# Kernel tuning notes

Measured on AMD Instinct MI355X. Metric: run time of the kernel, lower is better.

The kernel has to match this reference:

```python
import jax, jax.numpy as jnp
import numpy as np

B, S, H, NH = 2, 4096, 768, 12
DH = H // NH  # 64


def setup_inputs() -> dict:
    key = jax.random.key(0)
    ks = jax.random.split(key, 7)
    scale = 0.02
    return {
        "x": jax.random.normal(ks[0], (B, S, H), dtype=jnp.float32),
        "Wq": jax.random.normal(ks[1], (H, H), dtype=jnp.float32) * scale,
        "bq": jax.random.normal(ks[2], (H,), dtype=jnp.float32) * scale,
        "Wk": jax.random.normal(ks[3], (H, H), dtype=jnp.float32) * scale,
        "bk": jax.random.normal(ks[4], (H,), dtype=jnp.float32) * scale,
        "Wv": jax.random.normal(ks[5], (H, H), dtype=jnp.float32) * scale,
        "bv": jax.random.normal(ks[6], (H,), dtype=jnp.float32) * scale,
    }


def _split_heads(t):
    # [B,S,H] -> [B,NH,S,DH]
    return t.reshape(B, S, NH, DH).transpose(0, 2, 1, 3)


def reference(x, Wq, bq, Wk, bk, Wv, bv):
    q = _split_heads(x @ Wq + bq)
    k = _split_heads(x @ Wk + bk)
    v = _split_heads(x @ Wv + bv)
    # raw scores + zero additive mask (mask is all zeros, so it is a no-op)
    scores = jnp.einsum("bhqd,bhkd->bhqk", q, k) / jnp.sqrt(jnp.float32(DH))
    probs = jax.nn.softmax(scores, axis=-1)
    ctx = jnp.einsum("bhqk,bhkd->bhqd", probs, v)
    out = ctx.transpose(0, 2, 1, 3).reshape(B, S, H)
    return jnp.tanh(out)
```

## Files before the change

kernel.cpp:

```cpp
#include <hip/hip_runtime.h>
#include <hip/hip_bf16.h>

#define B_ 2
#define S_ 4096
#define H_ 768
#define NH_ 12
#define DH_ 64
#define M_ (B_ * S_)
#define N3_ (3 * H_)
#define NQK 1536
#define K_ H_
#define LOG2E 1.4426950408889634f

typedef __attribute__((ext_vector_type(8))) short short8;
typedef __attribute__((ext_vector_type(4))) float f32x4;
typedef __attribute__((ext_vector_type(16))) float f32x16;
typedef __attribute__((ext_vector_type(4))) unsigned int uint4v;
typedef __attribute__((ext_vector_type(4))) unsigned short ushort4v;

typedef __attribute__((address_space(3))) unsigned int lds_u32;
typedef const __attribute__((address_space(1))) unsigned int glb_u32;

__device__ __forceinline__ unsigned short f2bf(float f) {
    unsigned int u = __builtin_bit_cast(unsigned int, f);
    u += 0x7FFFu + ((u >> 16) & 1u);
    return (unsigned short)(u >> 16);
}
__device__ __forceinline__ unsigned int cvtpk_bf16(float lo, float hi) {
    unsigned int r;
    asm("v_cvt_pk_bf16_f32 %0, %1, %2" : "=v"(r) : "v"(lo), "v"(hi));
    return r;
}
__device__ __forceinline__ void plswap32(unsigned int &x, unsigned int &y) {
    asm("v_permlane32_swap_b32 %0, %1" : "+v"(x), "+v"(y));
}
__device__ __forceinline__ float exp2_fast(float x) {
    float r;
    asm("v_exp_f32 %0, %1" : "=v"(r) : "v"(x));
    return r;
}

__global__ __launch_bounds__(256) void cast_x_kernel(const float* __restrict__ x,
                                                     unsigned short* __restrict__ xb) {
    int i = blockIdx.x * 256 + threadIdx.x;
    float4 v = reinterpret_cast<const float4*>(x)[i];
    ushort4 o;
    o.x = f2bf(v.x); o.y = f2bf(v.y); o.z = f2bf(v.z); o.w = f2bf(v.w);
    reinterpret_cast<ushort4*>(xb)[i] = o;
}

__global__ __launch_bounds__(256) void cast_w_kernel(const float* __restrict__ Wq,
                                                     const float* __restrict__ Wk,
                                                     const float* __restrict__ Wv,
                                                     unsigned short* __restrict__ wt) {
    int id = blockIdx.x * 256 + threadIdx.x;
    int n = id % H_;
    int kb = (id / H_) % 96;
    int wsel = id / (H_ * 96);
    const float* W = (wsel == 0) ? Wq : (wsel == 1) ? Wk : Wv;
    union { unsigned short s[8]; uint4v v; } u;
#pragma unroll
    for (int j = 0; j < 8; j++) u.s[j] = f2bf(W[(size_t)(kb * 8 + j) * H_ + n]);
    *reinterpret_cast<uint4v*>(wt + (size_t)(wsel * H_ + n) * H_ + kb * 8) = u.v;
}

#define GBM 128
#define GBN 128
#define GBK 64

__global__ __launch_bounds__(256) void qkv_gemm_kernel(const unsigned short* __restrict__ xb,
                                                       const unsigned short* __restrict__ wt,
                                                       const float* __restrict__ bq,
                                                       const float* __restrict__ bk,
                                                       const float* __restrict__ bv,
                                                       unsigned short* __restrict__ qk,
                                                       unsigned short* __restrict__ vT) {
    __shared__ unsigned short Asm[GBM * GBK];
    __shared__ unsigned short Bsm[GBN * GBK];
    const int tid = threadIdx.x;
    const int swz = (blockIdx.x & 7) * 144 + (blockIdx.x >> 3);
    const int bm = swz / 18, bn = swz % 18;
    const int w = tid >> 6, l = tid & 63;
    const int wm = w >> 1, wn = w & 1;
    const int lr = l & 15, lk = l >> 4;

    f32x4 zero = {0.f, 0.f, 0.f, 0.f};
    f32x4 acc[4][4];
#pragma unroll
    for (int i = 0; i < 4; i++)
#pragma unroll
        for (int j = 0; j < 4; j++) acc[i][j] = zero;

    const int srow = l >> 3;
    const int scol = (l & 7) * 8;
    const unsigned short* aBase = xb + (size_t)(bm * GBM) * K_;
    const unsigned short* bBase = wt + (size_t)(bn * GBN) * K_;

    for (int k0 = 0; k0 < K_; k0 += GBK) {
        __syncthreads();
#pragma unroll
        for (int i = 0; i < 4; i++) {
            const int j = w * 4 + i;
            __builtin_amdgcn_global_load_lds(
                (glb_u32*)(aBase + (size_t)(j * 8 + srow) * K_ + k0 + scol),
                (lds_u32*)(&Asm[j * 8 * GBK]), 16, 0, 0);
        }
#pragma unroll
        for (int i = 0; i < 4; i++) {
            const int j = w * 4 + i;
            __builtin_amdgcn_global_load_lds(
                (glb_u32*)(bBase + (size_t)(j * 8 + srow) * K_ + k0 + scol),
                (lds_u32*)(&Bsm[j * 8 * GBK]), 16, 0, 0);
        }
        __syncthreads();

#pragma unroll
        for (int ks = 0; ks < 2; ks++) {
            short8 a[4], b[4];
#pragma unroll
            for (int mi = 0; mi < 4; mi++)
                a[mi] = *reinterpret_cast<const short8*>(&Asm[(wm * 64 + mi * 16 + lr) * GBK + ks * 32 + lk * 8]);
#pragma unroll
            for (int ni = 0; ni < 4; ni++)
                b[ni] = *reinterpret_cast<const short8*>(&Bsm[(wn * 64 + ni * 16 + lr) * GBK + ks * 32 + lk * 8]);
#pragma unroll
            for (int mi = 0; mi < 4; mi++)
#pragma unroll
                for (int ni = 0; ni < 4; ni++)
                    acc[mi][ni] = __builtin_amdgcn_mfma_f32_16x16x32_bf16(a[mi], b[ni], acc[mi][ni], 0, 0, 0);
        }
    }

    if (bn < 12) {
#pragma unroll
        for (int ni = 0; ni < 4; ni++) {
            const int col = bn * GBN + wn * 64 + ni * 16 + lr;
            const bool isQ = (col < H_);
            const float bias = isQ ? bq[col] : bk[col - H_];
            const float scl = isQ ? (0.125f * LOG2E) : 1.0f;
#pragma unroll
            for (int mi = 0; mi < 4; mi++) {
#pragma unroll
                for (int i = 0; i < 4; i++) {
                    const int row = bm * GBM + wm * 64 + mi * 16 + lk * 4 + i;
                    qk[(size_t)row * NQK + col] = f2bf((acc[mi][ni][i] + bias) * scl);
                }
            }
        }
    } else {
#pragma unroll
        for (int ni = 0; ni < 4; ni++) {
            const int c = bn * GBN - 2 * H_ + wn * 64 + ni * 16 + lr;
            const int h = c >> 6, d = c & 63;
            const float bias = bv[c];
#pragma unroll
            for (int mi = 0; mi < 4; mi++) {
                const int row0 = bm * GBM + wm * 64 + mi * 16 + lk * 4;
                const int b = row0 >> 12, s0 = row0 & (S_ - 1);
                union { unsigned short s[4]; ushort4v v; } u;
#pragma unroll
                for (int i = 0; i < 4; i++) u.s[i] = f2bf(acc[mi][ni][i] + bias);
                *reinterpret_cast<ushort4v*>(vT + ((size_t)(b * NH_ + h) * DH_ + d) * S_ + s0) = u.v;
            }
        }
    }
}

#define QW 32
#define QB 128
#define KB 64

__global__ __launch_bounds__(256, 2) void attn_kernel(const unsigned short* __restrict__ qk,
                                                      const unsigned short* __restrict__ vT,
                                                      float* __restrict__ out) {
    __shared__ unsigned short Ksm[KB * 64];
    __shared__ unsigned short Vsm[DH_ * KB];
    const int tid = threadIdx.x;
    const int w = tid >> 6, l = tid & 63;
    const int ln = l & 31, hi = l >> 5;
    const int swz = (blockIdx.x & 7) * 96 + (blockIdx.x >> 3);
    const int qt = swz & 31, bh = swz >> 5;
    const int b = bh / NH_, h = bh % NH_;

    const unsigned short* Qg = qk + (size_t)b * S_ * NQK + h * DH_;
    const unsigned short* Kg = Qg + H_;
    const unsigned short* Vg = vT + (size_t)bh * DH_ * S_;

    const int qrow = qt * QB + w * QW + ln;
    short8 qf[4];
    {
        const unsigned short* qp = Qg + (size_t)qrow * NQK + hi * 8;
#pragma unroll
        for (int dk = 0; dk < 4; dk++)
            qf[dk] = *reinterpret_cast<const short8*>(qp + dk * 16);
    }

    const f32x16 fz = {0,0,0,0,0,0,0,0,0,0,0,0,0,0,0,0};
    f32x16 o0 = fz, o1 = fz;
    float m_ = -INFINITY, lsum = 0.f;

    const int srow = tid >> 2;
    const int sd = (tid & 3) * 16;
    const unsigned short* kgp = Kg + (size_t)srow * NQK + sd;
    const unsigned short* vgp = Vg + (size_t)srow * S_ + sd;
    const int sidx0 = (srow * 64 + sd) ^ ((srow & 7) << 3);
    const int sidx1 = (srow * 64 + sd + 8) ^ ((srow & 7) << 3);

    uint4v kr0 = *reinterpret_cast<const uint4v*>(kgp);
    uint4v kr1 = *reinterpret_cast<const uint4v*>(kgp + 8);
    uint4v vr0 = *reinterpret_cast<const uint4v*>(vgp);
    uint4v vr1 = *reinterpret_cast<const uint4v*>(vgp + 8);

    for (int kt = 0; kt < S_; kt += KB) {
        asm volatile("" ::: "memory");
        __builtin_amdgcn_s_barrier();
        asm volatile("" ::: "memory");
        *reinterpret_cast<uint4v*>(&Ksm[sidx0]) = kr0;
        *reinterpret_cast<uint4v*>(&Ksm[sidx1]) = kr1;
        *reinterpret_cast<uint4v*>(&Vsm[sidx0]) = vr0;
        *reinterpret_cast<uint4v*>(&Vsm[sidx1]) = vr1;
        if (kt + KB < S_) {
            kr0 = *reinterpret_cast<const uint4v*>(kgp + (size_t)(kt + KB) * NQK);
            kr1 = *reinterpret_cast<const uint4v*>(kgp + (size_t)(kt + KB) * NQK + 8);
            vr0 = *reinterpret_cast<const uint4v*>(vgp + kt + KB);
            vr1 = *reinterpret_cast<const uint4v*>(vgp + kt + KB + 8);
        }
        asm volatile("s_waitcnt lgkmcnt(0)" ::: "memory");
        __builtin_amdgcn_s_barrier();
        asm volatile("" ::: "memory");

        f32x16 s0 = fz, s1 = fz;
#pragma unroll
        for (int dk = 0; dk < 4; dk++) {
            const int col = dk * 16 + hi * 8;
            short8 kf0 = *reinterpret_cast<const short8*>(&Ksm[(ln * 64 + col) ^ ((ln & 7) << 3)]);
            short8 kf1 = *reinterpret_cast<const short8*>(&Ksm[((32 + ln) * 64 + col) ^ ((ln & 7) << 3)]);
            s0 = __builtin_amdgcn_mfma_f32_32x32x16_bf16(kf0, qf[dk], s0, 0, 0, 0);
            s1 = __builtin_amdgcn_mfma_f32_32x32x16_bf16(kf1, qf[dk], s1, 0, 0, 0);
        }

        float pmax = fmaxf(fmaxf(s0[0], s0[1]), fmaxf(s0[2], s0[3]));
#pragma unroll
        for (int r = 4; r < 16; r += 4)
            pmax = fmaxf(pmax, fmaxf(fmaxf(s0[r], s0[r+1]), fmaxf(s0[r+2], s0[r+3])));
#pragma unroll
        for (int r = 0; r < 16; r += 4)
            pmax = fmaxf(pmax, fmaxf(fmaxf(s1[r], s1[r+1]), fmaxf(s1[r+2], s1[r+3])));
        pmax = fmaxf(pmax, __shfl_xor(pmax, 32));
        if (!__all(pmax - m_ <= 8.0f)) {
            const float mnew = fmaxf(m_, pmax);
            const float corr = exp2_fast(m_ - mnew);
            m_ = mnew;
            lsum *= corr;
#pragma unroll
            for (int r = 0; r < 16; r++) {
                const float c = __shfl(corr, (r & 3) + 8 * (r >> 2) + 4 * hi);
                o0[r] *= c; o1[r] *= c;
            }
        }
        float p[32];
        float rs = 0.f;
#pragma unroll
        for (int r = 0; r < 16; r++) { p[r] = exp2_fast(s0[r] - m_); rs += p[r]; }
#pragma unroll
        for (int r = 0; r < 16; r++) { p[16 + r] = exp2_fast(s1[r] - m_); rs += p[16 + r]; }
        rs += __shfl_xor(rs, 32);
        lsum += rs;

        short8 pa[4];
#pragma unroll
        for (int half = 0; half < 2; half++) {
            unsigned int c0 = cvtpk_bf16(p[half*16+0],  p[half*16+1]);
            unsigned int c1 = cvtpk_bf16(p[half*16+2],  p[half*16+3]);
            unsigned int c2 = cvtpk_bf16(p[half*16+4],  p[half*16+5]);
            unsigned int c3 = cvtpk_bf16(p[half*16+6],  p[half*16+7]);
            unsigned int c4 = cvtpk_bf16(p[half*16+8],  p[half*16+9]);
            unsigned int c5 = cvtpk_bf16(p[half*16+10], p[half*16+11]);
            unsigned int c6 = cvtpk_bf16(p[half*16+12], p[half*16+13]);
            unsigned int c7 = cvtpk_bf16(p[half*16+14], p[half*16+15]);
            plswap32(c0, c2); plswap32(c1, c3);
            plswap32(c4, c6); plswap32(c5, c7);
            union { unsigned int u[4]; short8 v; } ua, ub;
            ua.u[0] = c0; ua.u[1] = c1; ua.u[2] = c2; ua.u[3] = c3;
            ub.u[0] = c4; ub.u[1] = c5; ub.u[2] = c6; ub.u[3] = c7;
            pa[half * 2]     = ua.v;
            pa[half * 2 + 1] = ub.v;
        }

#pragma unroll
        for (int s4 = 0; s4 < 4; s4++) {
            const int kcol = s4 * 16 + hi * 8;
            short8 vf0 = *reinterpret_cast<const short8*>(&Vsm[(ln * 64 + kcol) ^ ((ln & 7) << 3)]);
            short8 vf1 = *reinterpret_cast<const short8*>(&Vsm[((32 + ln) * 64 + kcol) ^ ((ln & 7) << 3)]);
            o0 = __builtin_amdgcn_mfma_f32_32x32x16_bf16(pa[s4], vf0, o0, 0, 0, 0);
            o1 = __builtin_amdgcn_mfma_f32_32x32x16_bf16(pa[s4], vf1, o1, 0, 0, 0);
        }
    }

    float* op = out + ((size_t)b * S_ + qt * QB + w * QW) * H_ + h * DH_;
#pragma unroll
    for (int r = 0; r < 16; r++) {
        const int q = (r & 3) + 8 * (r >> 2) + 4 * hi;
        const float inv = 1.0f / __shfl(lsum, q);
        op[(size_t)q * H_ + ln]      = tanhf(o0[r] * inv);
        op[(size_t)q * H_ + 32 + ln] = tanhf(o1[r] * inv);
    }
}

extern "C" void kernel_launch(void* const* d_in, const int* in_sizes, int n_in,
                              void* d_out, int out_size, void* d_ws, size_t ws_size,
                              hipStream_t stream) {
    const float* x  = (const float*)d_in[0];
    const float* Wq = (const float*)d_in[1];
    const float* bq = (const float*)d_in[2];
    const float* Wk = (const float*)d_in[3];
    const float* bk = (const float*)d_in[4];
    const float* Wv = (const float*)d_in[5];
    const float* bv = (const float*)d_in[6];
    float* out = (float*)d_out;

    char* ws = (char*)d_ws;
    unsigned short* xb = (unsigned short*)ws;
    size_t off = (size_t)M_ * K_ * 2;
    unsigned short* wt = (unsigned short*)(ws + off);
    off += (size_t)N3_ * K_ * 2;
    unsigned short* qkb = (unsigned short*)(ws + off);
    off += (size_t)M_ * NQK * 2;
    unsigned short* vTb = (unsigned short*)(ws + off);

    cast_x_kernel<<<dim3((M_ * K_) / 4 / 256), dim3(256), 0, stream>>>(x, xb);
    cast_w_kernel<<<dim3((3 * H_ * 96) / 256), dim3(256), 0, stream>>>(Wq, Wk, Wv, wt);
    qkv_gemm_kernel<<<dim3((M_ / GBM) * (N3_ / GBN)), dim3(256), 0, stream>>>(xb, wt, bq, bk, bv, qkb, vTb);
    attn_kernel<<<dim3(B_ * NH_ * (S_ / QB)), dim3(256), 0, stream>>>(qkb, vTb, out);
}
```

Measured before the change: 284.3 us.

## Swizzle GEMM LDS tiles and fold running max into attention MFMA accumulator

The QKV projection GEMM now XOR-swizzles the 16-byte column slots of its LDS tiles by row, both on the global-to-LDS load and on the fragment reads, to cut LDS bank conflicts. In the attention loop the score accumulators start at -m, so the MFMA output is already max-shifted. This removes the 32 per-element subtractions before exp2 and simplifies the rescale test to pm <= 8. The running max now starts at 0 rather than -inf, which changes the numerical initialisation and could matter for inputs with very negative scores.

Result: faster. 270.8 us (-4.7%).

```diff
diff --git a/kernel.cpp b/kernel.cpp
--- a/kernel.cpp
+++ b/kernel.cpp
@@ -91,8 +91,8 @@
 #pragma unroll
         for (int j = 0; j < 4; j++) acc[i][j] = zero;
 
-    const int srow = l >> 3;
-    const int scol = (l & 7) * 8;
+    const int sr8 = l >> 3;
+    const int scolS = (((l & 7) ^ sr8) * 8);
     const unsigned short* aBase = xb + (size_t)(bm * GBM) * K_;
     const unsigned short* bBase = wt + (size_t)(bn * GBN) * K_;
 
@@ -102,14 +102,14 @@
         for (int i = 0; i < 4; i++) {
             const int j = w * 4 + i;
             __builtin_amdgcn_global_load_lds(
-                (glb_u32*)(aBase + (size_t)(j * 8 + srow) * K_ + k0 + scol),
+                (glb_u32*)(aBase + (size_t)(j * 8 + sr8) * K_ + k0 + scolS),
                 (lds_u32*)(&Asm[j * 8 * GBK]), 16, 0, 0);
         }
 #pragma unroll
         for (int i = 0; i < 4; i++) {
             const int j = w * 4 + i;
             __builtin_amdgcn_global_load_lds(
-                (glb_u32*)(bBase + (size_t)(j * 8 + srow) * K_ + k0 + scol),
+                (glb_u32*)(bBase + (size_t)(j * 8 + sr8) * K_ + k0 + scolS),
                 (lds_u32*)(&Bsm[j * 8 * GBK]), 16, 0, 0);
         }
         __syncthreads();
@@ -118,11 +118,17 @@
         for (int ks = 0; ks < 2; ks++) {
             short8 a[4], b[4];
 #pragma unroll
-            for (int mi = 0; mi < 4; mi++)
-                a[mi] = *reinterpret_cast<const short8*>(&Asm[(wm * 64 + mi * 16 + lr) * GBK + ks * 32 + lk * 8]);
-#pragma unroll
-            for (int ni = 0; ni < 4; ni++)
-                b[ni] = *reinterpret_cast<const short8*>(&Bsm[(wn * 64 + ni * 16 + lr) * GBK + ks * 32 + lk * 8]);
+            for (int mi = 0; mi < 4; mi++) {
+                const int row = wm * 64 + mi * 16 + lr;
+                const int slot = ((ks * 4 + lk) ^ (lr & 7)) * 8;
+                a[mi] = *reinterpret_cast<const short8*>(&Asm[row * GBK + slot]);
+            }
+#pragma unroll
+            for (int ni = 0; ni < 4; ni++) {
+                const int row = wn * 64 + ni * 16 + lr;
+                const int slot = ((ks * 4 + lk) ^ (lr & 7)) * 8;
+                b[ni] = *reinterpret_cast<const short8*>(&Bsm[row * GBK + slot]);
+            }
 #pragma unroll
             for (int mi = 0; mi < 4; mi++)
 #pragma unroll
@@ -197,7 +203,7 @@
 
     const f32x16 fz = {0,0,0,0,0,0,0,0,0,0,0,0,0,0,0,0};
     f32x16 o0 = fz, o1 = fz;
-    float m_ = -INFINITY, lsum = 0.f;
+    float m_ = 0.f, lsum = 0.f;
 
     const int srow = tid >> 2;
     const int sd = (tid & 3) * 16;
@@ -229,7 +235,10 @@
         __builtin_amdgcn_s_barrier();
         asm volatile("" ::: "memory");
 
-        f32x16 s0 = fz, s1 = fz;
+        f32x16 cm;
+#pragma unroll
+        for (int r = 0; r < 16; r++) cm[r] = -m_;
+        f32x16 s0 = cm, s1 = cm;
 #pragma unroll
         for (int dk = 0; dk < 4; dk++) {
             const int col = dk * 16 + hi * 8;
@@ -239,19 +248,21 @@
             s1 = __builtin_amdgcn_mfma_f32_32x32x16_bf16(kf1, qf[dk], s1, 0, 0, 0);
         }
 
-        float pmax = fmaxf(fmaxf(s0[0], s0[1]), fmaxf(s0[2], s0[3]));
-#pragma unroll
-        for (int r = 4; r < 16; r += 4)
-            pmax = fmaxf(pmax, fmaxf(fmaxf(s0[r], s0[r+1]), fmaxf(s0[r+2], s0[r+3])));
+        float pm = -1e30f;
 #pragma unroll
         for (int r = 0; r < 16; r += 4)
-            pmax = fmaxf(pmax, fmaxf(fmaxf(s1[r], s1[r+1]), fmaxf(s1[r+2], s1[r+3])));
-        pmax = fmaxf(pmax, __shfl_xor(pmax, 32));
-        if (!__all(pmax - m_ <= 8.0f)) {
-            const float mnew = fmaxf(m_, pmax);
-            const float corr = exp2_fast(m_ - mnew);
-            m_ = mnew;
+            pm = fmaxf(fmaxf(pm, s0[r]), fmaxf(fmaxf(s0[r+1], s0[r+2]), s0[r+3]));
+#pragma unroll
+        for (int r = 0; r < 16; r += 4)
+            pm = fmaxf(fmaxf(pm, s1[r]), fmaxf(fmaxf(s1[r+1], s1[r+2]), s1[r+3]));
+        pm = fmaxf(pm, __shfl_xor(pm, 32));
+        if (!__all(pm <= 8.0f)) {
+            const float step = fmaxf(pm, 0.f);
+            const float corr = exp2_fast(-step);
+            m_ += step;
             lsum *= corr;
+#pragma unroll
+            for (int r = 0; r < 16; r++) { s0[r] -= step; s1[r] -= step; }
 #pragma unroll
             for (int r = 0; r < 16; r++) {
                 const float c = __shfl(corr, (r & 3) + 8 * (r >> 2) + 4 * hi);
@@ -261,9 +272,9 @@
         float p[32];
         float rs = 0.f;
 #pragma unroll
-        for (int r = 0; r < 16; r++) { p[r] = exp2_fast(s0[r] - m_); rs += p[r]; }
-#pragma unroll
-        for (int r = 0; r < 16; r++) { p[16 + r] = exp2_fast(s1[r] - m_); rs += p[16 + r]; }
+        for (int r = 0; r < 16; r++) { p[r] = exp2_fast(s0[r]); rs += p[r]; }
+#pragma unroll
+        for (int r = 0; r < 16; r++) { p[16 + r] = exp2_fast(s1[r]); rs += p[16 + r]; }
         rs += __shfl_xor(rs, 32);
         lsum += rs;
 
```
